# Kernel tuning notes

Measured on AMD Instinct MI355X. Metric: run time of the kernel, lower is better.

The kernel has to match this reference:

```python
import jax, jax.numpy as jnp
import numpy as np

B, S, D, H, DFF = 2, 2048, 1024, 16, 4096
DK = D // H
EPS = 1e-6


def layer_norm(x, alpha, bias):
    # TF reduce_std is biased std; eps added to std (not variance)
    mean = jnp.mean(x, axis=-1, keepdims=True)
    std = jnp.sqrt(jnp.mean((x - mean) ** 2, axis=-1, keepdims=True))
    return alpha * (x - mean) / (std + EPS) + bias


def setup_inputs() -> dict:
    key = jax.random.key(0)
    ks = jax.random.split(key, 10)
    s = 0.02
    return {
        "x": jax.random.normal(ks[0], (B, S, D), jnp.float32),
        "mask": jnp.ones((B, 1, 1, S), jnp.int32),
        "wq": jax.random.normal(ks[1], (D, D), jnp.float32) * s,
        "wk": jax.random.normal(ks[2], (D, D), jnp.float32) * s,
        "wv": jax.random.normal(ks[3], (D, D), jnp.float32) * s,
        "wo": jax.random.normal(ks[4], (D, D), jnp.float32) * s,
        "w1": jax.random.normal(ks[5], (D, DFF), jnp.float32) * s,
        "b1": jnp.zeros((DFF,), jnp.float32),
        "w2": jax.random.normal(ks[6], (DFF, D), jnp.float32) * s,
        "b2": jnp.zeros((D,), jnp.float32),
        "ln1_a": jnp.ones((D,), jnp.float32),
        "ln1_b": jnp.zeros((D,), jnp.float32),
        "ln2_a": jnp.ones((D,), jnp.float32),
        "ln2_b": jnp.zeros((D,), jnp.float32),
    }


def reference(x, mask, wq, wk, wv, wo, w1, b1, w2, b2, ln1_a, ln1_b, ln2_a, ln2_b):
    # --- residual 1: pre-norm self-attention ---
    xn = layer_norm(x, ln1_a, ln1_b)
    q = (xn @ wq).reshape(B, S, H, DK)
    k = (xn @ wk).reshape(B, S, H, DK)
    v = (xn @ wv).reshape(B, S, H, DK)
    scores = jnp.einsum('bqhd,bkhd->bhqk', q, k) / jnp.sqrt(jnp.float32(DK))
    scores = jnp.where(mask == 0, jnp.float32(-1e9), scores)
    attn = jax.nn.softmax(scores, axis=-1)  # dropout = identity at eval
    ctx = jnp.einsum('bhqk,bkhd->bqhd', attn, v).reshape(B, S, D)
    x = x + ctx @ wo
    # --- residual 2: pre-norm FFN ---
    xn = layer_norm(x, ln2_a, ln2_b)
    ff = jax.nn.relu(xn @ w1 + b1) @ w2 + b2
    return x + ff
```

## Files before the change

kernel.cpp:

```cpp
#include <hip/hip_runtime.h>

#define BATCH 2
#define SEQ   2048
#define DMODEL 1024
#define NHEAD 16
#define DHEAD 64
#define DFF_  4096
#define MROWS (BATCH*SEQ)
#define EPS 1e-6f

typedef unsigned short u16;
typedef unsigned int u32;
typedef __bf16 bf16x8 __attribute__((ext_vector_type(8)));
typedef float  f32x4  __attribute__((ext_vector_type(4)));
typedef u32    u32x2  __attribute__((ext_vector_type(2)));

__device__ __forceinline__ float bf2f(u16 h) {
    union { u32 u; float f; } v; v.u = ((u32)h) << 16; return v.f;
}
__device__ __forceinline__ u16 f2bf(float f) {
    union { float f; u32 u; } v; v.f = f;
    u32 u = v.u;
    u32 r = (u + 0x7fffu + ((u >> 16) & 1u)) >> 16;
    return (u16)r;
}

__device__ __forceinline__ void async16(const u16* g, u16* l) {
    __builtin_amdgcn_global_load_lds((const __attribute__((address_space(1))) void*)g,
                                     (__attribute__((address_space(3))) void*)l,
                                     16, 0, 0);
}

__global__ __launch_bounds__(256) void transpose_all(
        const float* __restrict__ wq, const float* __restrict__ wk,
        const float* __restrict__ wv, const float* __restrict__ wo,
        const float* __restrict__ w1, const float* __restrict__ w2,
        u16* __restrict__ wqkvT, u16* __restrict__ woT,
        u16* __restrict__ w1T, u16* __restrict__ w2T) {
    __shared__ float tile[32][33];
    int id = blockIdx.x;
    const float* in; u16* out; int R, C, tx, ty;
    if (id < 4096) {
        int m = id >> 10, t2 = id & 1023;
        tx = t2 & 31; ty = t2 >> 5;
        R = DMODEL; C = DMODEL;
        switch (m) {
            case 0: in = wq; out = wqkvT;                 break;
            case 1: in = wk; out = wqkvT + 1024 * 1024;   break;
            case 2: in = wv; out = wqkvT + 2 * 1024 * 1024; break;
            default: in = wo; out = woT;                  break;
        }
    } else if (id < 8192) {
        int t2 = id - 4096;
        tx = t2 & 127; ty = t2 >> 7;
        R = DMODEL; C = DFF_;
        in = w1; out = w1T;
    } else {
        int t2 = id - 8192;
        tx = t2 & 31; ty = t2 >> 5;
        R = DFF_; C = DMODEL;
        in = w2; out = w2T;
    }
    int c0 = tx * 32, r0 = ty * 32;
    int x = threadIdx.x, y = threadIdx.y;
    #pragma unroll
    for (int i = 0; i < 32; i += 8)
        tile[y + i][x] = in[(size_t)(r0 + y + i) * C + c0 + x];
    __syncthreads();
    #pragma unroll
    for (int i = 0; i < 32; i += 8)
        out[(size_t)(c0 + y + i) * R + r0 + x] = f2bf(tile[x][y + i]);
}

__global__ __launch_bounds__(256) void transpose_v_perm(const u16* __restrict__ qkv,
                                                        u16* __restrict__ vtp) {
    __shared__ u16 tile[64][72];
    int kt = blockIdx.x * 64;
    int bh = blockIdx.y; int b = bh >> 4, h = bh & 15;
    const u16* in = qkv + ((size_t)(b * SEQ + kt)) * 3072 + 2 * DMODEL + h * DHEAD;
    u16* out = vtp + ((size_t)bh * DHEAD) * SEQ;
    int t = threadIdx.x;
    int r = t >> 3, c8 = (t & 7) * 8;
    #pragma unroll
    for (int pass = 0; pass < 2; pass++) {
        int row = r + pass * 32;
        uint4 v = *(const uint4*)(in + (size_t)row * 3072 + c8);
        *(uint4*)&tile[row][c8] = v;
    }
    __syncthreads();
    #pragma unroll
    for (int pass = 0; pass < 2; pass++) {
        int d = r + pass * 32;
        u16 o8[8];
        #pragma unroll
        for (int e = 0; e < 8; e++) {
            int c = c8 + e;
            o8[e] = tile[(c & 3) * 16 + (c >> 2)][d];
        }
        *(uint4*)(out + (size_t)d * SEQ + kt + c8) = *(const uint4*)o8;
    }
}

__global__ __launch_bounds__(256) void ln_kernel(const float* __restrict__ x,
                                                 const float* __restrict__ alpha,
                                                 const float* __restrict__ beta,
                                                 u16* __restrict__ out) {
    int row = blockIdx.x;
    int t = threadIdx.x;
    const float* xr = x + (size_t)row * DMODEL;
    float4 xv = ((const float4*)xr)[t];
    float f0 = xv.x, f1 = xv.y, f2 = xv.z, f3 = xv.w;
    float s1 = f0 + f1 + f2 + f3;
    float s2 = f0*f0 + f1*f1 + f2*f2 + f3*f3;
    #pragma unroll
    for (int off = 32; off >= 1; off >>= 1) {
        s1 += __shfl_xor(s1, off);
        s2 += __shfl_xor(s2, off);
    }
    __shared__ float r1[4], r2[4];
    int w = t >> 6, lane = t & 63;
    if (lane == 0) { r1[w] = s1; r2[w] = s2; }
    __syncthreads();
    s1 = r1[0] + r1[1] + r1[2] + r1[3];
    s2 = r2[0] + r2[1] + r2[2] + r2[3];
    float mean = s1 * (1.0f / DMODEL);
    float var  = s2 * (1.0f / DMODEL) - mean * mean;
    var = fmaxf(var, 0.0f);
    float inv = 1.0f / (sqrtf(var) + EPS);
    float4 av = ((const float4*)alpha)[t];
    float4 bv = ((const float4*)beta)[t];
    ushort4 ov;
    ov.x = f2bf(av.x * (f0 - mean) * inv + bv.x);
    ov.y = f2bf(av.y * (f1 - mean) * inv + bv.y);
    ov.z = f2bf(av.z * (f2 - mean) * inv + bv.z);
    ov.w = f2bf(av.w * (f3 - mean) * inv + bv.w);
    ((ushort4*)(out + (size_t)row * DMODEL))[t] = ov;
}

#define BK 64

template <int AI, int AJ, bool OUT_F32, bool SWAP = false>
__global__ __launch_bounds__(256) void gemm_bt(const u16* __restrict__ A,
                                               const u16* __restrict__ BT,
                                               void* __restrict__ Cp,
                                               const float* __restrict__ bias,
                                               const float* __restrict__ residual,
                                               int M, int N, int K, int do_relu) {
    constexpr int BMt = AI * 32, BNt = AJ * 32;
    __shared__ u16 As[BMt * BK];
    __shared__ u16 Bs[BNt * BK];
    int t = threadIdx.x;
    int bx = blockIdx.x;
    if ((gridDim.x & 7) == 0) {
        int cpx = gridDim.x >> 3;
        bx = (bx & 7) * cpx + (bx >> 3);
    }
    int mt = SWAP ? bx : (int)blockIdx.y;
    int nt = SWAP ? (int)blockIdx.y : bx;
    int m0 = mt * BMt, n0 = nt * BNt;
    int lane = t & 63, w = t >> 6;
    int wr = w >> 1, wc = w & 1;
    int lhi = lane >> 4, llo = lane & 15;
    int sr = lane >> 3, sk = lane & 7;
    int skx = (sk ^ sr) * 8;

    f32x4 acc[AI][AJ] = {};

    const u16* Ab = A  + (size_t)m0 * K + skx;
    const u16* Bb = BT + (size_t)n0 * K + skx;

    for (int k0 = 0; k0 < K; k0 += BK) {
        __syncthreads();
        #pragma unroll
        for (int j = 0; j < AI; j++) {
            int blk = w * AI + j;
            async16(Ab + (size_t)(blk * 8 + sr) * K + k0, &As[blk * 512]);
        }
        #pragma unroll
        for (int j = 0; j < AJ; j++) {
            int blk = w * AJ + j;
            async16(Bb + (size_t)(blk * 8 + sr) * K + k0, &Bs[blk * 512]);
        }
        __syncthreads();
        #pragma unroll
        for (int kk = 0; kk < 2; kk++) {
            int slot = ((kk * 4 + lhi) ^ (llo & 7)) * 8;
            bf16x8 af[AI], bfr[AJ];
            #pragma unroll
            for (int i = 0; i < AI; i++)
                af[i]  = *(const bf16x8*)(&As[(wr * 16 * AI + i * 16 + llo) * 64 + slot]);
            #pragma unroll
            for (int j = 0; j < AJ; j++)
                bfr[j] = *(const bf16x8*)(&Bs[(wc * 16 * AJ + j * 16 + llo) * 64 + slot]);
            #pragma unroll
            for (int i = 0; i < AI; i++)
                #pragma unroll
                for (int j = 0; j < AJ; j++)
                    acc[i][j] = __builtin_amdgcn_mfma_f32_16x16x32_bf16(af[i], bfr[j], acc[i][j], 0, 0, 0);
        }
    }

    #pragma unroll
    for (int i = 0; i < AI; i++) {
        #pragma unroll
        for (int rr = 0; rr < 4; rr++) {
            int row = m0 + wr * 16 * AI + i * 16 + lhi * 4 + rr;
            #pragma unroll
            for (int j = 0; j < AJ; j++) {
                int col = n0 + wc * 16 * AJ + j * 16 + llo;
                float v = acc[i][j][rr];
                if (bias)      v += bias[col];
                if (residual)  v += residual[(size_t)row * N + col];
                if (do_relu)   v = fmaxf(v, 0.0f);
                size_t idx = (size_t)row * N + col;
                if (OUT_F32) ((float*)Cp)[idx] = v;
                else         ((u16*)Cp)[idx]   = f2bf(v);
            }
        }
    }
}

#define SCL 0.18033688f

__global__ __launch_bounds__(256) void flash_attn(const u16* __restrict__ qkv,
                                                  const u16* __restrict__ vtp,
                                                  const int* __restrict__ mask,
                                                  u16* __restrict__ ctx) {
    __shared__ u16 QPs[64 * 64];
    __shared__ u16 Ks[64 * 64];
    __shared__ u16 VTs[64 * 64];
    __shared__ float mbias[64];

    int t = threadIdx.x;
    int w = t >> 6, lane = t & 63, lhi = lane >> 4, llo = lane & 15;
    int sr = lane >> 3, sk = lane & 7;
    int skx = (sk ^ sr) * 8;

    int f  = (blockIdx.z * NHEAD + blockIdx.y) * (SEQ / 64) + blockIdx.x;
    int s  = f & 31;
    int q0 = (f >> 5) * 64;
    int hb = (s & 7) * 4 + (s >> 3);
    int h = hb & 15, b = hb >> 4;

    const u16* Qg  = qkv + ((size_t)(b * SEQ + q0)) * 3072 + h * DHEAD;
    const u16* Kg  = qkv + ((size_t)(b * SEQ)) * 3072 + DMODEL + h * DHEAD;
    const u16* VTg = vtp + ((size_t)((b * NHEAD + h) * DHEAD)) * SEQ;

    #pragma unroll
    for (int j = 0; j < 2; j++) {
        int blk = w * 2 + j;
        async16(Qg + (size_t)(blk * 8 + sr) * 3072 + skx, &QPs[blk * 512]);
    }
    __syncthreads();
    bf16x8 qf[2];
    #pragma unroll
    for (int kk = 0; kk < 2; kk++)
        qf[kk] = *(const bf16x8*)&QPs[(w * 16 + llo) * 64 + ((kk * 4 + lhi) ^ (llo & 7)) * 8];

    u16* Ps = QPs + w * 1024;

    float l_part[4] = {};
    f32x4 o_acc[4] = {};

    for (int kt = 0; kt < SEQ; kt += 64) {
        __syncthreads();
        #pragma unroll
        for (int j = 0; j < 2; j++) {
            int blk = w * 2 + j;
            async16(Kg  + (size_t)(kt + blk * 8 + sr) * 3072 + skx, &Ks[blk * 512]);
            async16(VTg + (size_t)(blk * 8 + sr) * SEQ + kt + skx,  &VTs[blk * 512]);
        }
        if (t < 64) mbias[t] = (mask[b * SEQ + kt + t] == 0) ? -1.0e12f : 0.0f;
        __syncthreads();

        f32x4 s4[4] = {};
        __builtin_amdgcn_s_setprio(1);
        #pragma unroll
        for (int kk = 0; kk < 2; kk++) {
            #pragma unroll
            for (int j = 0; j < 4; j++) {
                bf16x8 kf = *(const bf16x8*)&Ks[(j * 16 + llo) * 64 +
                                                ((kk * 4 + lhi) ^ (llo & 7)) * 8];
                s4[j] = __builtin_amdgcn_mfma_f32_16x16x32_bf16(qf[kk], kf, s4[j], 0, 0, 0);
            }
        }
        __builtin_amdgcn_s_setprio(0);
        float mb[4];
        #pragma unroll
        for (int j = 0; j < 4; j++) mb[j] = mbias[j * 16 + llo];

        #pragma unroll
        for (int rr = 0; rr < 4; rr++) {
            u32 pu[4];
            #pragma unroll
            for (int j = 0; j < 4; j++) {
                float p = __builtin_amdgcn_exp2f(__builtin_fmaf(s4[j][rr], SCL, mb[j]));
                l_part[rr] += p;
                union { float f; u32 u; } c; c.f = p;
                pu[j] = c.u;
            }
            u32x2 pw;
            pw[0] = (pu[0] >> 16) | (pu[1] & 0xffff0000u);
            pw[1] = (pu[2] >> 16) | (pu[3] & 0xffff0000u);
            int prow = lhi * 4 + rr;
            *(u32x2*)&Ps[prow * 64 + ((llo >> 1) ^ (prow & 7)) * 8 + (llo & 1) * 4] = pw;
        }
        __builtin_amdgcn_s_setprio(1);
        #pragma unroll
        for (int kk = 0; kk < 2; kk++) {
            bf16x8 pf = *(const bf16x8*)&Ps[llo * 64 + ((kk * 4 + lhi) ^ (llo & 7)) * 8];
            #pragma unroll
            for (int nb = 0; nb < 4; nb++) {
                bf16x8 vf = *(const bf16x8*)&VTs[(nb * 16 + llo) * 64 +
                                                 ((kk * 4 + lhi) ^ (llo & 7)) * 8];
                o_acc[nb] = __builtin_amdgcn_mfma_f32_16x16x32_bf16(pf, vf, o_acc[nb], 0, 0, 0);
            }
        }
        __builtin_amdgcn_s_setprio(0);
    }

    #pragma unroll
    for (int rr = 0; rr < 4; rr++) {
        float l = l_part[rr];
        #pragma unroll
        for (int off = 1; off <= 8; off <<= 1) l += __shfl_xor(l, off);
        float inv = __builtin_amdgcn_rcpf(l);
        int row = q0 + w * 16 + lhi * 4 + rr;
        #pragma unroll
        for (int nb = 0; nb < 4; nb++) {
            int col = h * DHEAD + nb * 16 + llo;
            ctx[((size_t)(b * SEQ) + row) * DMODEL + col] = f2bf(o_acc[nb][rr] * inv);
        }
    }
}

extern "C" void kernel_launch(void* const* d_in, const int* in_sizes, int n_in,
                              void* d_out, int out_size, void* d_ws, size_t ws_size,
                              hipStream_t stream) {
    (void)in_sizes; (void)n_in; (void)out_size; (void)ws_size;
    const float* x    = (const float*)d_in[0];
    const int* mask   = (const int*)d_in[1];
    const float* wq   = (const float*)d_in[2];
    const float* wk   = (const float*)d_in[3];
    const float* wv   = (const float*)d_in[4];
    const float* wo   = (const float*)d_in[5];
    const float* w1   = (const float*)d_in[6];
    const float* b1   = (const float*)d_in[7];
    const float* w2   = (const float*)d_in[8];
    const float* b2   = (const float*)d_in[9];
    const float* ln1a = (const float*)d_in[10];
    const float* ln1b = (const float*)d_in[11];
    const float* ln2a = (const float*)d_in[12];
    const float* ln2b = (const float*)d_in[13];
    float* out = (float*)d_out;

    char* wsb = (char*)d_ws;
    const size_t MB = 1024 * 1024;
    u16*   wqkvT = (u16*)(wsb + 0);
    u16*   woT   = (u16*)(wsb + 6 * MB);
    u16*   w1T   = (u16*)(wsb + 8 * MB);
    u16*   w2T   = (u16*)(wsb + 16 * MB);
    u16*   xn    = (u16*)(wsb + 24 * MB);
    float* x2    = (float*)(wsb + 32 * MB);
    u16*   vtp   = (u16*)(wsb + 32 * MB);
    u16*   ctx   = (u16*)(wsb + 48 * MB);
    u16*   qkv   = (u16*)(wsb + 56 * MB);
    u16*   ff1   = (u16*)(wsb + 56 * MB);

    transpose_all<<<12288, dim3(32, 8), 0, stream>>>(
        wq, wk, wv, wo, w1, w2,
        wqkvT, woT, w1T, w2T);

    ln_kernel<<<MROWS, 256, 0, stream>>>(x, ln1a, ln1b, xn);
    gemm_bt<4,2,false><<<dim3(3072/64, MROWS/128), 256, 0, stream>>>(xn, wqkvT, qkv,
                                                                     nullptr, nullptr,
                                                                     MROWS, 3072, DMODEL, 0);
    transpose_v_perm<<<dim3(SEQ/64, BATCH*NHEAD), 256, 0, stream>>>(qkv, vtp);
    flash_attn<<<dim3(SEQ/64, NHEAD, BATCH), 256, 0, stream>>>(qkv, vtp, mask, ctx);
    gemm_bt<2,2,true,true><<<dim3(MROWS/64, DMODEL/64), 256, 0, stream>>>(
        ctx, woT, x2, nullptr, x, MROWS, DMODEL, DMODEL, 0);
    ln_kernel<<<MROWS, 256, 0, stream>>>(x2, ln2a, ln2b, xn);
    gemm_bt<4,2,false><<<dim3(DFF_/64, MROWS/128), 256, 0, stream>>>(xn, w1T, ff1,
                                                                    b1, nullptr,
                                                                    MROWS, DFF_, DMODEL, 1);
    gemm_bt<2,2,true,true><<<dim3(MROWS/64, DMODEL/64), 256, 0, stream>>>(
        ff1, w2T, out, b2, x2, MROWS, DMODEL, DFF_, 0);
}
```

Before: 357.8 us.

## Split attention key range in two and combine partial outputs

Each attention block now handles only half of the key sequence, which doubles the grid to expose more parallelism per query tile. Each half writes its normalized partial context in bf16 plus its row sums. A new combine kernel reweights the two halves by those row sums into the final context. The cost is an extra kernel launch, extra global traffic for the partial outputs, and additional bf16 rounding of the intermediate results.

```diff
diff --git a/kernel.cpp b/kernel.cpp
--- a/kernel.cpp
+++ b/kernel.cpp
@@ -225,7 +225,9 @@
 __global__ __launch_bounds__(256) void flash_attn(const u16* __restrict__ qkv,
                                                   const u16* __restrict__ vtp,
                                                   const int* __restrict__ mask,
-                                                  u16* __restrict__ ctx) {
+                                                  u16* __restrict__ po0,
+                                                  u16* __restrict__ po1,
+                                                  float* __restrict__ pl) {
     __shared__ u16 QPs[64 * 64];
     __shared__ u16 Ks[64 * 64];
     __shared__ u16 VTs[64 * 64];
@@ -237,10 +239,11 @@
     int skx = (sk ^ sr) * 8;
 
     int f  = (blockIdx.z * NHEAD + blockIdx.y) * (SEQ / 64) + blockIdx.x;
-    int s  = f & 31;
-    int q0 = (f >> 5) * 64;
-    int hb = (s & 7) * 4 + (s >> 3);
-    int h = hb & 15, b = hb >> 4;
+    int q0 = (f >> 6) * 64;
+    int r  = f & 63;
+    int u  = (r & 7) * 8 + (r >> 3);
+    int b = u >> 5, h = (u >> 1) & 15, half = u & 1;
+    int kbase = half * (SEQ / 2);
 
     const u16* Qg  = qkv + ((size_t)(b * SEQ + q0)) * 3072 + h * DHEAD;
     const u16* Kg  = qkv + ((size_t)(b * SEQ)) * 3072 + DMODEL + h * DHEAD;
@@ -262,7 +265,7 @@
     float l_part[4] = {};
     f32x4 o_acc[4] = {};
 
-    for (int kt = 0; kt < SEQ; kt += 64) {
+    for (int kt = kbase; kt < kbase + SEQ / 2; kt += 64) {
         __syncthreads();
         #pragma unroll
         for (int j = 0; j < 2; j++) {
@@ -319,6 +322,7 @@
         __builtin_amdgcn_s_setprio(0);
     }
 
+    u16* po = half ? po1 : po0;
     #pragma unroll
     for (int rr = 0; rr < 4; rr++) {
         float l = l_part[rr];
@@ -329,9 +333,32 @@
         #pragma unroll
         for (int nb = 0; nb < 4; nb++) {
             int col = h * DHEAD + nb * 16 + llo;
-            ctx[((size_t)(b * SEQ) + row) * DMODEL + col] = f2bf(o_acc[nb][rr] * inv);
-        }
-    }
+            po[((size_t)(b * SEQ) + row) * DMODEL + col] = f2bf(o_acc[nb][rr] * inv);
+        }
+        if (llo == 0)
+            pl[(((size_t)half * BATCH + b) * NHEAD + h) * SEQ + row] = l;
+    }
+}
+
+__global__ __launch_bounds__(256) void attn_combine(u16* po0,
+                                                    const u16* __restrict__ po1,
+                                                    const float* __restrict__ pl) {
+    int row = blockIdx.x;
+    int b = row >> 11, seq = row & (SEQ - 1);
+    int t = threadIdx.x;
+    int h = t >> 4;
+    float l0 = pl[(((size_t)0 * BATCH + b) * NHEAD + h) * SEQ + seq];
+    float l1 = pl[(((size_t)1 * BATCH + b) * NHEAD + h) * SEQ + seq];
+    float inv = __builtin_amdgcn_rcpf(l0 + l1);
+    float w0 = l0 * inv, w1 = l1 * inv;
+    ushort4 a = ((const ushort4*)(po0 + (size_t)row * DMODEL))[t];
+    ushort4 c = ((const ushort4*)(po1 + (size_t)row * DMODEL))[t];
+    ushort4 o;
+    o.x = f2bf(bf2f(a.x) * w0 + bf2f(c.x) * w1);
+    o.y = f2bf(bf2f(a.y) * w0 + bf2f(c.y) * w1);
+    o.z = f2bf(bf2f(a.z) * w0 + bf2f(c.z) * w1);
+    o.w = f2bf(bf2f(a.w) * w0 + bf2f(c.w) * w1);
+    ((ushort4*)(po0 + (size_t)row * DMODEL))[t] = o;
 }
 
 extern "C" void kernel_launch(void* const* d_in, const int* in_sizes, int n_in,
@@ -361,8 +388,10 @@
     u16*   w1T   = (u16*)(wsb + 8 * MB);
     u16*   w2T   = (u16*)(wsb + 16 * MB);
     u16*   xn    = (u16*)(wsb + 24 * MB);
+    float* pl    = (float*)(wsb + 24 * MB);
     float* x2    = (float*)(wsb + 32 * MB);
     u16*   vtp   = (u16*)(wsb + 32 * MB);
+    u16*   po1   = (u16*)(wsb + 40 * MB);
     u16*   ctx   = (u16*)(wsb + 48 * MB);
     u16*   qkv   = (u16*)(wsb + 56 * MB);
     u16*   ff1   = (u16*)(wsb + 56 * MB);
@@ -376,7 +405,9 @@
                                                                      nullptr, nullptr,
                                                                      MROWS, 3072, DMODEL, 0);
     transpose_v_perm<<<dim3(SEQ/64, BATCH*NHEAD), 256, 0, stream>>>(qkv, vtp);
-    flash_attn<<<dim3(SEQ/64, NHEAD, BATCH), 256, 0, stream>>>(qkv, vtp, mask, ctx);
+    flash_attn<<<dim3(SEQ/64, NHEAD, BATCH*2), 256, 0, stream>>>(qkv, vtp, mask,
+                                                                 ctx, po1, pl);
+    attn_combine<<<MROWS, 256, 0, stream>>>(ctx, po1, pl);
     gemm_bt<2,2,true,true><<<dim3(MROWS/64, DMODEL/64), 256, 0, stream>>>(
         ctx, woT, x2, nullptr, x, MROWS, DMODEL, DMODEL, 0);
     ln_kernel<<<MROWS, 256, 0, stream>>>(x2, ln2a, ln2b, xn);
```

Measured after the change: 380.6 us. 6.4% more time.
